# Kernel optimization log

Hardware: AMD Instinct MI355X
Metric: run time of the kernel (lower is better)

The kernel has to match this reference:

```python
import jax, jax.numpy as jnp
import numpy as np
import math

N = 50000
E = 800000
C_IN = 32
C_H = 256
C_OUT = 3
DEPTH = 3
RATIO = 0.5


def setup_inputs() -> dict:
    key = jax.random.key(0)
    ks = jax.random.split(key, 16)
    s = 0.05  # keep tanh/relu in a healthy range
    f32 = jnp.float32
    return {
        "x": jax.random.normal(ks[0], (N, C_IN), f32),
        "edge_index": jax.random.randint(ks[1], (2, E), 0, N, jnp.int32).astype(jnp.int64),
        "w0_l": jax.random.normal(ks[2], (C_IN, C_H), f32) * s,
        "w0_r": jax.random.normal(ks[3], (C_IN, C_H), f32) * s,
        "b0": jax.random.normal(ks[4], (C_H,), f32) * s,
        "dwl": jax.random.normal(ks[5], (DEPTH, C_H, C_H), f32) * s,
        "dwr": jax.random.normal(ks[6], (DEPTH, C_H, C_H), f32) * s,
        "db": jax.random.normal(ks[7], (DEPTH, C_H), f32) * s,
        "pool_w": jax.random.normal(ks[8], (DEPTH, C_H), f32),
        "uwl": jax.random.normal(ks[9], (DEPTH - 1, C_H, C_H), f32) * s,
        "uwr": jax.random.normal(ks[10], (DEPTH - 1, C_H, C_H), f32) * s,
        "ub": jax.random.normal(ks[11], (DEPTH - 1, C_H), f32) * s,
        "uwl_last": jax.random.normal(ks[12], (C_H, C_OUT), f32) * s,
        "uwr_last": jax.random.normal(ks[13], (C_H, C_OUT), f32) * s,
        "ub_last": jax.random.normal(ks[14], (C_OUT,), f32) * s,
    }


def _sage_max(x, src, dst, n, wl, wr, b):
    # SAGEConv(aggr='max'): out = lin_l(max_j x_j) + lin_r(x_i)
    # dst may contain dummy index n (masked edges); slice it off.
    msg = x[src]                                            # [E, C]
    agg = jax.ops.segment_max(msg, dst, num_segments=n + 1)[:n]
    agg = jnp.where(jnp.isfinite(agg), agg, 0.0)            # empty segments -> 0 (PyG)
    return agg @ wl + b + x @ wr


def _topk_pool(x, src, dst, w, ratio):
    # PyG TopKPooling with min_score=None: score=tanh((x.w)/||w||), keep top-k, rescale.
    n = x.shape[0]
    k = math.ceil(ratio * n)
    score = jnp.tanh((x @ w) / jnp.linalg.norm(w))          # [n]
    vals, perm = jax.lax.top_k(score, k)
    x2 = x[perm] * vals[:, None]
    # relabel edges; dropped edges -> dummy node k (fixed shape, equivalent for max-agg)
    mapping = jnp.full((n + 1,), -1, jnp.int32).at[perm].set(jnp.arange(k, dtype=jnp.int32))
    nsrc, ndst = mapping[src], mapping[dst]
    valid = (nsrc >= 0) & (ndst >= 0)
    src2 = jnp.where(valid, nsrc, 0)
    dst2 = jnp.where(valid, ndst, k)
    return x2, src2, dst2, perm, k


def reference(x, edge_index, w0_l, w0_r, b0, dwl, dwr, db, pool_w,
              uwl, uwr, ub, uwl_last, uwr_last, ub_last):
    n = x.shape[0]
    src = edge_index[0].astype(jnp.int32)
    dst = edge_index[1].astype(jnp.int32)

    x = jax.nn.relu(_sage_max(x, src, dst, n, w0_l, w0_r, b0))
    xs, srcs, dsts, ns, perms = [x], [src], [dst], [n], []

    for i in range(DEPTH):
        x, src, dst, perm, n = _topk_pool(x, src, dst, pool_w[i], RATIO)
        x = jax.nn.relu(_sage_max(x, src, dst, n, dwl[i], dwr[i], db[i]))
        if i < DEPTH - 1:
            xs.append(x); srcs.append(src); dsts.append(dst); ns.append(n)
        perms.append(perm)

    for i in range(DEPTH):
        j = DEPTH - 1 - i
        res, src, dst, n, perm = xs[j], srcs[j], dsts[j], ns[j], perms[j]
        up = jnp.zeros_like(res).at[perm].set(x)
        x = res + up                                         # sum_res=True
        if i < DEPTH - 1:
            x = jax.nn.relu(_sage_max(x, src, dst, n, uwl[i], uwr[i], ub[i]))
        else:
            x = _sage_max(x, src, dst, n, uwl_last, uwr_last, ub_last)

    return jnp.tanh(x) * 0.5
```

## Files before the change

### kernel.cpp

```cpp
#include <hip/hip_runtime.h>
#include <math.h>

#define E_NUM 800000
#define CH 256

typedef __attribute__((ext_vector_type(8))) short short8;
typedef __attribute__((ext_vector_type(4))) float float4v;

__device__ __forceinline__ unsigned f2key(float s) {
  unsigned b = __float_as_uint(s);
  return (b & 0x80000000u) ? ~b : (b | 0x80000000u);
}


__global__ __launch_bounds__(256) void k_deg(const int* __restrict__ dst, int n,
                                             int* __restrict__ deg) {
  int e = blockIdx.x * 256 + threadIdx.x;
  if (e < E_NUM) { int d = dst[e]; if (d < n) atomicAdd(&deg[d], 1); }
}

__global__ __launch_bounds__(256) void k_scan_block(const int* __restrict__ deg, int n,
                                                    int* __restrict__ incl,
                                                    int* __restrict__ bsum) {
  __shared__ int s[256];
  int i = blockIdx.x * 256 + threadIdx.x;
  int v = (i < n) ? deg[i] : 0;
  s[threadIdx.x] = v;
  __syncthreads();
  for (int o = 1; o < 256; o <<= 1) {
    int t = (threadIdx.x >= o) ? s[threadIdx.x - o] : 0;
    __syncthreads();
    s[threadIdx.x] += t;
    __syncthreads();
  }
  if (i < n) incl[i] = s[threadIdx.x];
  if (threadIdx.x == 255) bsum[blockIdx.x] = s[255];
}

__global__ void k_scan_bsum(int* bsum, int nb, int* total_out) {
  if (threadIdx.x == 0 && blockIdx.x == 0) {
    int acc = 0;
    for (int b = 0; b < nb; b++) { int v = bsum[b]; bsum[b] = acc; acc += v; }
    total_out[0] = acc;
  }
}

__global__ __launch_bounds__(256) void k_scan_final(const int* __restrict__ deg,
                                                    const int* __restrict__ incl,
                                                    const int* __restrict__ bsum, int n,
                                                    int* __restrict__ row,
                                                    int* __restrict__ cursor) {
  int i = blockIdx.x * 256 + threadIdx.x;
  if (i < n) {
    int r = incl[i] - deg[i] + bsum[blockIdx.x];
    row[i] = r;
    cursor[i] = r;
  }
}

__global__ __launch_bounds__(256) void k_fill(const int* __restrict__ src,
                                              const int* __restrict__ dst, int n,
                                              int* __restrict__ cursor,
                                              int* __restrict__ col) {
  int e = blockIdx.x * 256 + threadIdx.x;
  if (e < E_NUM) {
    int d = dst[e];
    if (d < n) { int p = atomicAdd(&cursor[d], 1); col[p] = src[e]; }
  }
}

__global__ __launch_bounds__(256) void k_relabel_deg(const int* __restrict__ srcIn,
                                                     const int* __restrict__ dstIn,
                                                     const int* __restrict__ mapping,
                                                     int kNew, int* __restrict__ srcOut,
                                                     int* __restrict__ dstOut,
                                                     int* __restrict__ deg) {
  int e = blockIdx.x * 256 + threadIdx.x;
  if (e >= E_NUM) return;
  int ns = mapping[srcIn[e]];
  int nd = mapping[dstIn[e]];
  if (ns >= 0 && nd >= 0) {
    srcOut[e] = ns;
    dstOut[e] = nd;
    atomicAdd(&deg[nd], 1);
  } else {
    srcOut[e] = 0;
    dstOut[e] = kNew;
  }
}


__device__ __forceinline__ float4 fmax4(float4 a, float4 b) {
  return make_float4(fmaxf(a.x, b.x), fmaxf(a.y, b.y), fmaxf(a.z, b.z), fmaxf(a.w, b.w));
}

__global__ __launch_bounds__(256) void k_aggmax32(const float* __restrict__ x,
                                                  const int* __restrict__ row,
                                                  const int* __restrict__ col,
                                                  float* __restrict__ out, int n) {
  int node = blockIdx.x * 8 + threadIdx.x / 32;
  int c = threadIdx.x % 32;
  if (node >= n) return;
  int e0 = row[node], e1 = row[node + 1];
  float m0 = -INFINITY, m1 = -INFINITY, m2 = -INFINITY, m3 = -INFINITY;
  int e = e0;
  for (; e + 4 <= e1; e += 4) {
    int s0 = col[e], s1 = col[e + 1], s2 = col[e + 2], s3 = col[e + 3];
    float v0 = x[(size_t)s0 * 32 + c];
    float v1 = x[(size_t)s1 * 32 + c];
    float v2 = x[(size_t)s2 * 32 + c];
    float v3 = x[(size_t)s3 * 32 + c];
    m0 = fmaxf(m0, v0); m1 = fmaxf(m1, v1); m2 = fmaxf(m2, v2); m3 = fmaxf(m3, v3);
  }
  for (; e < e1; e++) m0 = fmaxf(m0, x[(size_t)col[e] * 32 + c]);
  float m = fmaxf(fmaxf(m0, m1), fmaxf(m2, m3));
  out[(size_t)node * 32 + c] = (e1 > e0) ? m : 0.0f;
}

__global__ __launch_bounds__(256) void k_aggmax4(const float* __restrict__ x,
                                                 const int* __restrict__ row,
                                                 const int* __restrict__ col,
                                                 float* __restrict__ out, int n) {
  int lane = threadIdx.x & 63;
  int node = blockIdx.x * 4 + (threadIdx.x >> 6);
  if (node >= n) return;
  int e0 = row[node], e1 = row[node + 1];
  float4 m0 = make_float4(-INFINITY, -INFINITY, -INFINITY, -INFINITY);
  float4 m1 = m0, m2 = m0, m3 = m0;
  int e = e0;
  for (; e + 4 <= e1; e += 4) {
    int s0 = col[e], s1 = col[e + 1], s2 = col[e + 2], s3 = col[e + 3];
    float4 v0 = *(const float4*)&x[(size_t)s0 * CH + lane * 4];
    float4 v1 = *(const float4*)&x[(size_t)s1 * CH + lane * 4];
    float4 v2 = *(const float4*)&x[(size_t)s2 * CH + lane * 4];
    float4 v3 = *(const float4*)&x[(size_t)s3 * CH + lane * 4];
    m0 = fmax4(m0, v0); m1 = fmax4(m1, v1); m2 = fmax4(m2, v2); m3 = fmax4(m3, v3);
  }
  for (; e < e1; e++)
    m0 = fmax4(m0, *(const float4*)&x[(size_t)col[e] * CH + lane * 4]);
  float4 m = fmax4(fmax4(m0, m1), fmax4(m2, m3));
  if (e1 <= e0) m = make_float4(0.f, 0.f, 0.f, 0.f);
  *(float4*)&out[(size_t)node * CH + lane * 4] = m;
}

__device__ __forceinline__ float b2f(unsigned short s) {
  return __uint_as_float(((unsigned)s) << 16);
}
__device__ __forceinline__ float4 bmax4(float4 m, ushort4 v) {
  m.x = fmaxf(m.x, b2f(v.x));
  m.y = fmaxf(m.y, b2f(v.y));
  m.z = fmaxf(m.z, b2f(v.z));
  m.w = fmaxf(m.w, b2f(v.w));
  return m;
}

__global__ __launch_bounds__(256) void k_aggmax4_b16(const unsigned short* __restrict__ xb,
                                                     const int* __restrict__ row,
                                                     const int* __restrict__ col,
                                                     float* __restrict__ out, int n) {
  int lane = threadIdx.x & 63;
  int node = blockIdx.x * 4 + (threadIdx.x >> 6);
  if (node >= n) return;
  int e0 = row[node], e1 = row[node + 1];
  float4 m0 = make_float4(-INFINITY, -INFINITY, -INFINITY, -INFINITY);
  float4 m1 = m0, m2 = m0, m3 = m0;
  int e = e0;
  for (; e + 4 <= e1; e += 4) {
    int s0 = col[e], s1 = col[e + 1], s2 = col[e + 2], s3 = col[e + 3];
    ushort4 v0 = *(const ushort4*)&xb[(size_t)s0 * CH + lane * 4];
    ushort4 v1 = *(const ushort4*)&xb[(size_t)s1 * CH + lane * 4];
    ushort4 v2 = *(const ushort4*)&xb[(size_t)s2 * CH + lane * 4];
    ushort4 v3 = *(const ushort4*)&xb[(size_t)s3 * CH + lane * 4];
    m0 = bmax4(m0, v0); m1 = bmax4(m1, v1); m2 = bmax4(m2, v2); m3 = bmax4(m3, v3);
  }
  for (; e < e1; e++)
    m0 = bmax4(m0, *(const ushort4*)&xb[(size_t)col[e] * CH + lane * 4]);
  float4 m = fmax4(fmax4(m0, m1), fmax4(m2, m3));
  if (e1 <= e0) m = make_float4(0.f, 0.f, 0.f, 0.f);
  *(float4*)&out[(size_t)node * CH + lane * 4] = m;
}


__global__ __launch_bounds__(256) void k_wprep(const float* __restrict__ src,
                                               unsigned short* __restrict__ dst, int K,
                                               int nmat) {
  int idx = blockIdx.x * 256 + threadIdx.x;
  int total = nmat * K * 256;
  if (idx >= total) return;
  int n = idx % 256;
  int k = (idx / 256) % K;
  int m = idx / (256 * K);
  float v = src[idx];
  unsigned u = __float_as_uint(v);
  unsigned h = u & 0xFFFF0000u;
  float r = v - __uint_as_float(h);
  unsigned short hs = (unsigned short)(h >> 16);
  unsigned short ls = (unsigned short)(__float_as_uint(r) >> 16);
  int ib = k >> 5, kk = k & 31;
  size_t base = (size_t)m * 2 * K * 256;
  size_t o = ((size_t)ib * 256 + n) * 32 + kk;
  dst[base + o] = hs;
  dst[base + (size_t)K * 256 + o] = ls;
}


#define KSTR 40

__global__ __launch_bounds__(256) void k_gemm_mfma(
    const float* __restrict__ A1, const float* __restrict__ A2,
    const unsigned short* __restrict__ W1t, const unsigned short* __restrict__ W2t,
    const float* __restrict__ bias, float* __restrict__ out, int M, int K, int scatter,
    const int* __restrict__ perm, const float* __restrict__ scw,
    float* __restrict__ score, unsigned* __restrict__ hist1) {
  __shared__ unsigned short As_h[64 * KSTR], As_l[64 * KSTR];
  __shared__ unsigned short Bs_h[256 * KSTR], Bs_l[256 * KSTR];
  __shared__ float sred[4][64];
  const int t = threadIdx.x;
  const int wave = t >> 6, lane = t & 63;
  const int l15 = lane & 15, qd = lane >> 4;
  const int bm0 = blockIdx.x * 64;
  float4v acc[4][4];
#pragma unroll
  for (int a = 0; a < 4; a++)
#pragma unroll
    for (int b = 0; b < 4; b++) acc[a][b] = (float4v)0.f;
  const int sa_m = t >> 2;
  const int sa_kc = (t & 3) * 8;
  const int rok = (bm0 + sa_m) < M;
  const int nIb = K >> 5;
  for (int ib = 0; ib < 2 * nIb; ib++) {
    const float* A = (ib < nIb) ? A1 : A2;
    const unsigned short* Wt = (ib < nIb) ? W1t : W2t;
    int ib0 = (ib < nIb) ? ib : ib - nIb;
    float va[8];
    {
      const float* ap = &A[(size_t)(bm0 + sa_m) * K + (ib0 << 5) + sa_kc];
      float4 v0 = rok ? *(const float4*)ap : make_float4(0, 0, 0, 0);
      float4 v1 = rok ? *(const float4*)(ap + 4) : make_float4(0, 0, 0, 0);
      va[0] = v0.x; va[1] = v0.y; va[2] = v0.z; va[3] = v0.w;
      va[4] = v1.x; va[5] = v1.y; va[6] = v1.z; va[7] = v1.w;
    }
    unsigned hp[4], lp[4];
#pragma unroll
    for (int e = 0; e < 4; e++) {
      unsigned u0 = __float_as_uint(va[2 * e]);
      unsigned u1 = __float_as_uint(va[2 * e + 1]);
      unsigned h0 = u0 & 0xFFFF0000u, h1 = u1 & 0xFFFF0000u;
      float r0 = va[2 * e] - __uint_as_float(h0);
      float r1 = va[2 * e + 1] - __uint_as_float(h1);
      hp[e] = (h0 >> 16) | h1;
      lp[e] = (__float_as_uint(r0) >> 16) | (__float_as_uint(r1) & 0xFFFF0000u);
    }
    size_t ro = ((size_t)ib0 * 256 + t) * 32;
    uint4 bh0 = *(const uint4*)&Wt[ro];
    uint4 bh1 = *(const uint4*)&Wt[ro + 8];
    uint4 bh2 = *(const uint4*)&Wt[ro + 16];
    uint4 bh3 = *(const uint4*)&Wt[ro + 24];
    size_t rl = (size_t)K * 256 + ro;
    uint4 bl0 = *(const uint4*)&Wt[rl];
    uint4 bl1 = *(const uint4*)&Wt[rl + 8];
    uint4 bl2 = *(const uint4*)&Wt[rl + 16];
    uint4 bl3 = *(const uint4*)&Wt[rl + 24];
    __syncthreads();
    *(uint4*)&As_h[sa_m * KSTR + sa_kc] = make_uint4(hp[0], hp[1], hp[2], hp[3]);
    *(uint4*)&As_l[sa_m * KSTR + sa_kc] = make_uint4(lp[0], lp[1], lp[2], lp[3]);
    *(uint4*)&Bs_h[t * KSTR + 0] = bh0;
    *(uint4*)&Bs_h[t * KSTR + 8] = bh1;
    *(uint4*)&Bs_h[t * KSTR + 16] = bh2;
    *(uint4*)&Bs_h[t * KSTR + 24] = bh3;
    *(uint4*)&Bs_l[t * KSTR + 0] = bl0;
    *(uint4*)&Bs_l[t * KSTR + 8] = bl1;
    *(uint4*)&Bs_l[t * KSTR + 16] = bl2;
    *(uint4*)&Bs_l[t * KSTR + 24] = bl3;
    __syncthreads();
    short8 ah[4], al[4], bh[4], bl[4];
#pragma unroll
    for (int mt = 0; mt < 4; mt++) {
      int r = (mt * 16 + l15) * KSTR + qd * 8;
      ah[mt] = *(const short8*)&As_h[r];
      al[mt] = *(const short8*)&As_l[r];
    }
#pragma unroll
    for (int nt = 0; nt < 4; nt++) {
      int r = (wave * 64 + nt * 16 + l15) * KSTR + qd * 8;
      bh[nt] = *(const short8*)&Bs_h[r];
      bl[nt] = *(const short8*)&Bs_l[r];
    }
#pragma unroll
    for (int mt = 0; mt < 4; mt++)
#pragma unroll
      for (int nt = 0; nt < 4; nt++) {
        acc[mt][nt] =
            __builtin_amdgcn_mfma_f32_16x16x32_bf16(ah[mt], bh[nt], acc[mt][nt], 0, 0, 0);
        acc[mt][nt] =
            __builtin_amdgcn_mfma_f32_16x16x32_bf16(ah[mt], bl[nt], acc[mt][nt], 0, 0, 0);
        acc[mt][nt] =
            __builtin_amdgcn_mfma_f32_16x16x32_bf16(al[mt], bh[nt], acc[mt][nt], 0, 0, 0);
      }
  }
  const int col0 = wave * 64;
  if (scw) {
    if (t < 64) { sred[0][t] = 0.f; sred[1][t] = 0.f; sred[2][t] = 0.f; sred[3][t] = 0.f; }
    __syncthreads();
  }
#pragma unroll
  for (int mt = 0; mt < 4; mt++) {
    int rbase = mt * 16 + qd * 4;
    float sp[4] = {0.f, 0.f, 0.f, 0.f};
#pragma unroll
    for (int nt = 0; nt < 4; nt++) {
      int col = col0 + nt * 16 + l15;
      float bb = bias[col];
      float wc = scw ? scw[col] : 0.f;
#pragma unroll
      for (int r = 0; r < 4; r++) {
        int p = bm0 + rbase + r;
        if (p < M) {
          float v = fmaxf(acc[mt][nt][r] + bb, 0.f);
          if (scatter) {
            float* dp = &out[(size_t)perm[p] * CH + col];
            *dp += v;
          } else {
            out[(size_t)p * CH + col] = v;
            sp[r] += v * wc;
          }
        }
      }
    }
    if (scw) {
#pragma unroll
      for (int r = 0; r < 4; r++) {
        float s = sp[r];
#pragma unroll
        for (int o = 1; o < 16; o <<= 1) s += __shfl_xor(s, o);
        if (l15 == 0) sred[wave][rbase + r] = s;
      }
    }
  }
  if (scw) {
    __syncthreads();
    if (t < 64 && bm0 + t < M) {
      float s = sred[0][t] + sred[1][t] + sred[2][t] + sred[3][t];
      score[bm0 + t] = s;
      atomicAdd(&hist1[f2key(s) >> 16], 1u);
    }
  }
}


__global__ __launch_bounds__(1024) void k_resolve(const unsigned* __restrict__ hist,
                                                  unsigned* __restrict__ state, int pass,
                                                  int k0) {
  __shared__ unsigned csum[1024];
  int t = threadIdx.x;
  int base = 65535 - 64 * t;
  unsigned s = 0;
  for (int j = 0; j < 64; j++) s += hist[base - j];
  csum[t] = s;
  __syncthreads();
  for (int o = 1; o < 1024; o <<= 1) {
    unsigned v = (t >= o) ? csum[t - o] : 0u;
    __syncthreads();
    csum[t] += v;
    __syncthreads();
  }
  unsigned cumBefore = csum[t] - s;
  unsigned kneed = (pass == 0) ? (unsigned)k0 : state[5];
  if (cumBefore < kneed && kneed <= cumBefore + s) {
    unsigned cum = cumBefore;
    for (int j = 0; j < 64; j++) {
      unsigned c = hist[base - j];
      if (cum + c >= kneed) {
        unsigned bucket = (unsigned)(base - j);
        if (pass == 0) {
          state[4] = bucket;
          state[5] = kneed - cum;
        } else {
          state[0] = (state[4] << 16) | bucket;
          state[1] = kneed - cum;
          state[2] = 0u;
          state[3] = 0u;
        }
        break;
      }
      cum += c;
    }
  }
}

__global__ __launch_bounds__(256) void k_hist2(const float* __restrict__ score, int n,
                                               const unsigned* __restrict__ state,
                                               unsigned* __restrict__ hist2) {
  int i = blockIdx.x * 256 + threadIdx.x;
  if (i >= n) return;
  unsigned u = f2key(score[i]);
  if ((u >> 16) == state[4]) atomicAdd(&hist2[u & 0xFFFFu], 1u);
}

__global__ __launch_bounds__(256) void k_compact(const float* __restrict__ score, int n,
                                                 unsigned* __restrict__ state,
                                                 int* __restrict__ perm,
                                                 int* __restrict__ mapping) {
  int i = blockIdx.x * 256 + threadIdx.x;
  if (i > n) return;
  if (i == n) { mapping[n] = -1; return; }
  unsigned Kth = state[0];
  unsigned kneed = state[1];
  unsigned u = f2key(score[i]);
  int m = -1;
  if (u > Kth) {
    unsigned p = atomicAdd(&state[2], 1u);
    perm[p] = i;
    m = (int)p;
  } else if (u == Kth) {
    unsigned tt = atomicAdd(&state[3], 1u);
    if (tt < kneed) {
      unsigned p = atomicAdd(&state[2], 1u);
      perm[p] = i;
      m = (int)p;
    }
  }
  mapping[i] = m;
}

__global__ __launch_bounds__(256) void k_gather(const float* __restrict__ x,
                                                const int* __restrict__ perm,
                                                const float* __restrict__ score,
                                                const float* __restrict__ pw,
                                                float* __restrict__ out, int k) {
  int lane = threadIdx.x & 63;
  int node = blockIdx.x * 4 + (threadIdx.x >> 6);
  float4 w4 = *(const float4*)&pw[lane * 4];
  float nn = w4.x * w4.x + w4.y * w4.y + w4.z * w4.z + w4.w * w4.w;
#pragma unroll
  for (int o = 32; o > 0; o >>= 1) nn += __shfl_down(nn, o);
  nn = __shfl(nn, 0);
  if (node >= k) return;
  int i = perm[node];
  float tv = tanhf(score[i] / sqrtf(nn));
  float4 v = *(const float4*)&x[(size_t)i * CH + lane * 4];
  v.x *= tv; v.y *= tv; v.z *= tv; v.w *= tv;
  *(float4*)&out[(size_t)node * CH + lane * 4] = v;
}


__device__ __forceinline__ unsigned short f2b_rn(float f) {
  unsigned u = __float_as_uint(f);
  u += 0x7FFFu + ((u >> 16) & 1u);
  return (unsigned short)(u >> 16);
}

__global__ __launch_bounds__(256) void k_cvtb16(const float* __restrict__ x,
                                                unsigned short* __restrict__ xb, int n) {
  int lane = threadIdx.x & 63;
  int node = blockIdx.x * 4 + (threadIdx.x >> 6);
  if (node >= n) return;
  float4 a = *(const float4*)&x[(size_t)node * CH + lane * 4];
  ushort4 o;
  o.x = f2b_rn(a.x); o.y = f2b_rn(a.y); o.z = f2b_rn(a.z); o.w = f2b_rn(a.w);
  *(ushort4*)&xb[(size_t)node * CH + lane * 4] = o;
}

__global__ __launch_bounds__(256) void k_final(const unsigned short* __restrict__ XB,
                                               const int* __restrict__ row,
                                               const int* __restrict__ col,
                                               const float* __restrict__ wl,
                                               const float* __restrict__ wr,
                                               const float* __restrict__ b,
                                               float* __restrict__ out, int n) {
  int lane = threadIdx.x & 63;
  int node = blockIdx.x * 4 + (threadIdx.x >> 6);
  if (node >= n) return;
  int e0 = row[node], e1 = row[node + 1];
  float4 m0 = make_float4(-INFINITY, -INFINITY, -INFINITY, -INFINITY);
  float4 m1 = m0, m2 = m0, m3 = m0;
  int e = e0;
  for (; e + 4 <= e1; e += 4) {
    int s0 = col[e], s1 = col[e + 1], s2 = col[e + 2], s3 = col[e + 3];
    ushort4 v0 = *(const ushort4*)&XB[(size_t)s0 * CH + lane * 4];
    ushort4 v1 = *(const ushort4*)&XB[(size_t)s1 * CH + lane * 4];
    ushort4 v2 = *(const ushort4*)&XB[(size_t)s2 * CH + lane * 4];
    ushort4 v3 = *(const ushort4*)&XB[(size_t)s3 * CH + lane * 4];
    m0 = bmax4(m0, v0); m1 = bmax4(m1, v1); m2 = bmax4(m2, v2); m3 = bmax4(m3, v3);
  }
  for (; e < e1; e++)
    m0 = bmax4(m0, *(const ushort4*)&XB[(size_t)col[e] * CH + lane * 4]);
  float4 m = fmax4(fmax4(m0, m1), fmax4(m2, m3));
  if (e1 <= e0) m = make_float4(0.f, 0.f, 0.f, 0.f);
  ushort4 sv4 = *(const ushort4*)&XB[(size_t)node * CH + lane * 4];
  float wlv[12], wrv[12];
  *(float4*)&wlv[0] = ((const float4*)(wl + 12 * lane))[0];
  *(float4*)&wlv[4] = ((const float4*)(wl + 12 * lane))[1];
  *(float4*)&wlv[8] = ((const float4*)(wl + 12 * lane))[2];
  *(float4*)&wrv[0] = ((const float4*)(wr + 12 * lane))[0];
  *(float4*)&wrv[4] = ((const float4*)(wr + 12 * lane))[1];
  *(float4*)&wrv[8] = ((const float4*)(wr + 12 * lane))[2];
  float av[4] = {m.x, m.y, m.z, m.w};
  float sv[4] = {b2f(sv4.x), b2f(sv4.y), b2f(sv4.z), b2f(sv4.w)};
  float p[3] = {0.f, 0.f, 0.f};
#pragma unroll
  for (int q = 0; q < 4; q++)
#pragma unroll
    for (int jj = 0; jj < 3; jj++)
      p[jj] += av[q] * wlv[q * 3 + jj] + sv[q] * wrv[q * 3 + jj];
#pragma unroll
  for (int jj = 0; jj < 3; jj++) {
#pragma unroll
    for (int o = 32; o > 0; o >>= 1) p[jj] += __shfl_down(p[jj], o);
  }
  if (lane == 0) {
#pragma unroll
    for (int jj = 0; jj < 3; jj++)
      out[(size_t)node * 3 + jj] = tanhf(p[jj] + b[jj]) * 0.5f;
  }
}


extern "C" void kernel_launch(void* const* d_in, const int* in_sizes, int n_in,
                              void* d_out, int out_size, void* d_ws, size_t ws_size,
                              hipStream_t stream) {
  (void)in_sizes; (void)n_in; (void)out_size; (void)ws_size;
  const float* xin = (const float*)d_in[0];
  const int* ei = (const int*)d_in[1];
  const int* src0 = ei;
  const int* dst0 = ei + E_NUM;
  const float* w0l = (const float*)d_in[2];
  const float* w0r = (const float*)d_in[3];
  const float* b0 = (const float*)d_in[4];
  const float* dwl = (const float*)d_in[5];
  const float* dwr = (const float*)d_in[6];
  const float* db = (const float*)d_in[7];
  const float* poolw = (const float*)d_in[8];
  const float* uwl = (const float*)d_in[9];
  const float* uwr = (const float*)d_in[10];
  const float* ub = (const float*)d_in[11];
  const float* uwlL = (const float*)d_in[12];
  const float* uwrL = (const float*)d_in[13];
  const float* ubL = (const float*)d_in[14];
  float* out = (float*)d_out;

  char* base = (char*)d_ws;
  size_t off = 0;
  auto alloc = [&](size_t bytes) -> void* {
    void* p = base + off;
    off = (off + bytes + 255) & ~(size_t)255;
    return p;
  };

  const int n0 = 50000, n1 = 25000, n2 = 12500, n3 = 6250;
  float* X0 = (float*)alloc((size_t)n0 * CH * 4);
  float* X1 = (float*)alloc((size_t)n1 * CH * 4);
  float* X2 = (float*)alloc((size_t)n2 * CH * 4);
  float* AGG = (float*)alloc((size_t)n1 * CH * 4);
  float* PD = (float*)alloc((size_t)n1 * CH * 4);
  unsigned short* XB = (unsigned short*)alloc((size_t)n0 * CH * 2);
  unsigned short* X1B = (unsigned short*)alloc((size_t)n1 * CH * 2);
  unsigned short* X2B = (unsigned short*)alloc((size_t)n2 * CH * 2);
  int* eA = (int*)alloc((size_t)2 * E_NUM * 4);
  int* eB = (int*)alloc((size_t)2 * E_NUM * 4);
  int* col0 = (int*)alloc((size_t)E_NUM * 4);
  int* col1 = (int*)alloc((size_t)E_NUM * 4);
  int* col2 = (int*)alloc((size_t)E_NUM * 4);
  int* col3 = (int*)alloc((size_t)E_NUM * 4);
  int* row0 = (int*)alloc((size_t)(n0 + 1) * 4);
  int* row1 = (int*)alloc((size_t)(n1 + 1) * 4);
  int* row2 = (int*)alloc((size_t)(n2 + 1) * 4);
  int* row3 = (int*)alloc((size_t)(n3 + 1) * 4);
  int* map1 = (int*)alloc((size_t)(n0 + 1) * 4);
  int* map2 = (int*)alloc((size_t)(n1 + 1) * 4);
  int* map3 = (int*)alloc((size_t)(n2 + 1) * 4);
  int* perm1 = (int*)alloc((size_t)n1 * 4);
  int* perm2 = (int*)alloc((size_t)n2 * 4);
  int* perm3 = (int*)alloc((size_t)n3 * 4);
  float* score = (float*)alloc((size_t)n0 * 4);
  int* deg = (int*)alloc((size_t)n0 * 4);
  int* incl = (int*)alloc((size_t)n0 * 4);
  int* cursor = (int*)alloc((size_t)n0 * 4);
  int* bsum = (int*)alloc((size_t)256 * 4);
  unsigned* state = (unsigned*)alloc(1024);
  unsigned* hist = (unsigned*)alloc((size_t)2 * 65536 * 4);
  const size_t WSZ = (size_t)2 * 256 * 256;
  unsigned short* Wt0l = (unsigned short*)alloc((size_t)2 * 32 * 256 * 2);
  unsigned short* Wt0r = (unsigned short*)alloc((size_t)2 * 32 * 256 * 2);
  unsigned short* Wtdl = (unsigned short*)alloc(3 * WSZ * 2);
  unsigned short* Wtdr = (unsigned short*)alloc(3 * WSZ * 2);
  unsigned short* Wtul = (unsigned short*)alloc(2 * WSZ * 2);
  unsigned short* Wtur = (unsigned short*)alloc(2 * WSZ * 2);

  const int EG = (E_NUM + 255) / 256;

  k_wprep<<<(32 * 256 + 255) / 256, 256, 0, stream>>>(w0l, Wt0l, 32, 1);
  k_wprep<<<(32 * 256 + 255) / 256, 256, 0, stream>>>(w0r, Wt0r, 32, 1);
  k_wprep<<<(3 * 256 * 256 + 255) / 256, 256, 0, stream>>>(dwl, Wtdl, 256, 3);
  k_wprep<<<(3 * 256 * 256 + 255) / 256, 256, 0, stream>>>(dwr, Wtdr, 256, 3);
  k_wprep<<<(2 * 256 * 256 + 255) / 256, 256, 0, stream>>>(uwl, Wtul, 256, 2);
  k_wprep<<<(2 * 256 * 256 + 255) / 256, 256, 0, stream>>>(uwr, Wtur, 256, 2);

  auto csrRest = [&](const int* esrc, const int* edst, int n, int* rowp, int* colp) {
    int nb = (n + 255) / 256;
    k_scan_block<<<nb, 256, 0, stream>>>(deg, n, incl, bsum);
    k_scan_bsum<<<1, 1, 0, stream>>>(bsum, nb, rowp + n);
    k_scan_final<<<nb, 256, 0, stream>>>(deg, incl, bsum, n, rowp, cursor);
    k_fill<<<EG, 256, 0, stream>>>(esrc, edst, n, cursor, colp);
  };

  auto poolLevel = [&](const float* X, const float* pw, int n, int k, int* mapping,
                       int* permL, const int* esrcIn, const int* edstIn, int* esrcOut,
                       int* edstOut, float* Pout) {
    k_resolve<<<1, 1024, 0, stream>>>(hist, state, 0, k);
    k_hist2<<<(n + 255) / 256, 256, 0, stream>>>(score, n, state, hist + 65536);
    k_resolve<<<1, 1024, 0, stream>>>(hist + 65536, state, 1, k);
    k_compact<<<(n + 1 + 255) / 256, 256, 0, stream>>>(score, n, state, permL, mapping);
    k_gather<<<(k + 3) / 4, 256, 0, stream>>>(X, permL, score, pw, Pout, k);
    hipMemsetAsync(deg, 0, (size_t)k * 4, stream);
    k_relabel_deg<<<EG, 256, 0, stream>>>(esrcIn, edstIn, mapping, k, esrcOut, edstOut,
                                          deg);
  };

  auto gemm = [&](const float* A1, const float* A2, const unsigned short* W1t,
                  const unsigned short* W2t, const float* bias, float* o, int M, int K,
                  int scatter, const int* prm, const float* scw, float* sc) {
    if (scw) hipMemsetAsync(hist, 0, (size_t)2 * 65536 * 4, stream);
    k_gemm_mfma<<<(M + 63) / 64, 256, 0, stream>>>(A1, A2, W1t, W2t, bias, o, M, K,
                                                   scatter, prm, scw, sc, hist);
  };

  hipMemsetAsync(deg, 0, (size_t)n0 * 4, stream);
  k_deg<<<EG, 256, 0, stream>>>(dst0, n0, deg);
  csrRest(src0, dst0, n0, row0, col0);
  k_aggmax32<<<(n0 + 7) / 8, 256, 0, stream>>>(xin, row0, col0, AGG, n0);
  gemm(AGG, xin, Wt0l, Wt0r, b0, X0, n0, 32, 0, nullptr, poolw + 0 * CH, score);

  poolLevel(X0, poolw + 0 * CH, n0, n1, map1, perm1, src0, dst0, eA, eA + E_NUM, PD);
  csrRest(eA, eA + E_NUM, n1, row1, col1);
  k_aggmax4<<<(n1 + 3) / 4, 256, 0, stream>>>(PD, row1, col1, AGG, n1);
  gemm(AGG, PD, Wtdl + 0 * WSZ, Wtdr + 0 * WSZ, db + 0 * CH, X1, n1, 256, 0, nullptr,
       poolw + 1 * CH, score);

  poolLevel(X1, poolw + 1 * CH, n1, n2, map2, perm2, eA, eA + E_NUM, eB, eB + E_NUM, PD);
  csrRest(eB, eB + E_NUM, n2, row2, col2);
  k_aggmax4<<<(n2 + 3) / 4, 256, 0, stream>>>(PD, row2, col2, AGG, n2);
  gemm(AGG, PD, Wtdl + 1 * WSZ, Wtdr + 1 * WSZ, db + 1 * CH, X2, n2, 256, 0, nullptr,
       poolw + 2 * CH, score);

  poolLevel(X2, poolw + 2 * CH, n2, n3, map3, perm3, eB, eB + E_NUM, eA, eA + E_NUM, PD);
  csrRest(eA, eA + E_NUM, n3, row3, col3);
  k_aggmax4<<<(n3 + 3) / 4, 256, 0, stream>>>(PD, row3, col3, AGG, n3);
  gemm(AGG, PD, Wtdl + 2 * WSZ, Wtdr + 2 * WSZ, db + 2 * CH, X2, n3, 256, 1, perm3,
       nullptr, nullptr);

  k_cvtb16<<<(n2 + 3) / 4, 256, 0, stream>>>(X2, X2B, n2);
  k_aggmax4_b16<<<(n2 + 3) / 4, 256, 0, stream>>>(X2B, row2, col2, AGG, n2);
  gemm(AGG, X2, Wtul + 0 * WSZ, Wtur + 0 * WSZ, ub + 0 * CH, X1, n2, 256, 1, perm2,
       nullptr, nullptr);

  k_cvtb16<<<(n1 + 3) / 4, 256, 0, stream>>>(X1, X1B, n1);
  k_aggmax4_b16<<<(n1 + 3) / 4, 256, 0, stream>>>(X1B, row1, col1, AGG, n1);
  gemm(AGG, X1, Wtul + 1 * WSZ, Wtur + 1 * WSZ, ub + 1 * CH, X0, n1, 256, 1, perm1,
       nullptr, nullptr);

  k_cvtb16<<<(n0 + 3) / 4, 256, 0, stream>>>(X0, XB, n0);
  k_final<<<(n0 + 3) / 4, 256, 0, stream>>>(XB, row0, col0, uwlL, uwrL, ubL, out, n0);
}
```

Before: 973.1 us.

## Compact surviving edges after pooling and vectorize GEMM epilogue stores

Edge relabeling now appends only surviving edges to the output arrays, using a global atomic counter. Later CSR fill and relabel kernels read that device-side count and exit early for edges beyond it, so dropped edges are no longer processed at deeper levels. Separately, the MFMA operands are swapped so each lane holds four consecutive output columns. This lets the GEMM epilogue load bias and score weights as float4, use float4 stores and read-modify-writes, and shrink the score reduction to two shuffles. The trade-off is a contended single-address atomic for edge compaction and grids still sized for the full edge count.

```diff
diff --git a/kernel.cpp b/kernel.cpp
--- a/kernel.cpp
+++ b/kernel.cpp
@@ -59,33 +59,36 @@
 }
 
 __global__ __launch_bounds__(256) void k_fill(const int* __restrict__ src,
-                                              const int* __restrict__ dst, int n,
+                                              const int* __restrict__ dst,
+                                              const int* __restrict__ ecnt,
                                               int* __restrict__ cursor,
                                               int* __restrict__ col) {
   int e = blockIdx.x * 256 + threadIdx.x;
-  if (e < E_NUM) {
-    int d = dst[e];
-    if (d < n) { int p = atomicAdd(&cursor[d], 1); col[p] = src[e]; }
-  }
+  int ne = ecnt ? *ecnt : E_NUM;
+  if (e >= ne) return;
+  int d = dst[e];
+  int p = atomicAdd(&cursor[d], 1);
+  col[p] = src[e];
 }
 
 __global__ __launch_bounds__(256) void k_relabel_deg(const int* __restrict__ srcIn,
                                                      const int* __restrict__ dstIn,
+                                                     const int* __restrict__ ecntIn,
                                                      const int* __restrict__ mapping,
-                                                     int kNew, int* __restrict__ srcOut,
+                                                     int* __restrict__ srcOut,
                                                      int* __restrict__ dstOut,
-                                                     int* __restrict__ deg) {
+                                                     int* __restrict__ deg,
+                                                     int* __restrict__ ecntOut) {
   int e = blockIdx.x * 256 + threadIdx.x;
-  if (e >= E_NUM) return;
+  int ne = ecntIn ? *ecntIn : E_NUM;
+  if (e >= ne) return;
   int ns = mapping[srcIn[e]];
   int nd = mapping[dstIn[e]];
   if (ns >= 0 && nd >= 0) {
-    srcOut[e] = ns;
-    dstOut[e] = nd;
+    int p = atomicAdd(ecntOut, 1);
+    srcOut[p] = ns;
+    dstOut[p] = nd;
     atomicAdd(&deg[nd], 1);
-  } else {
-    srcOut[e] = 0;
-    dstOut[e] = kNew;
   }
 }
 
@@ -291,11 +294,11 @@
 #pragma unroll
       for (int nt = 0; nt < 4; nt++) {
         acc[mt][nt] =
-            __builtin_amdgcn_mfma_f32_16x16x32_bf16(ah[mt], bh[nt], acc[mt][nt], 0, 0, 0);
+            __builtin_amdgcn_mfma_f32_16x16x32_bf16(bh[nt], ah[mt], acc[mt][nt], 0, 0, 0);
         acc[mt][nt] =
-            __builtin_amdgcn_mfma_f32_16x16x32_bf16(ah[mt], bl[nt], acc[mt][nt], 0, 0, 0);
+            __builtin_amdgcn_mfma_f32_16x16x32_bf16(bl[nt], ah[mt], acc[mt][nt], 0, 0, 0);
         acc[mt][nt] =
-            __builtin_amdgcn_mfma_f32_16x16x32_bf16(al[mt], bh[nt], acc[mt][nt], 0, 0, 0);
+            __builtin_amdgcn_mfma_f32_16x16x32_bf16(bh[nt], al[mt], acc[mt][nt], 0, 0, 0);
       }
   }
   const int col0 = wave * 64;
@@ -303,38 +306,51 @@
     if (t < 64) { sred[0][t] = 0.f; sred[1][t] = 0.f; sred[2][t] = 0.f; sred[3][t] = 0.f; }
     __syncthreads();
   }
+  float bias4[4][4], scw4[4][4];
+#pragma unroll
+  for (int nt = 0; nt < 4; nt++) {
+    int cb = col0 + nt * 16 + qd * 4;
+    *(float4*)bias4[nt] = *(const float4*)&bias[cb];
+    if (scw) *(float4*)scw4[nt] = *(const float4*)&scw[cb];
+  }
 #pragma unroll
   for (int mt = 0; mt < 4; mt++) {
-    int rbase = mt * 16 + qd * 4;
-    float sp[4] = {0.f, 0.f, 0.f, 0.f};
-#pragma unroll
-    for (int nt = 0; nt < 4; nt++) {
-      int col = col0 + nt * 16 + l15;
-      float bb = bias[col];
-      float wc = scw ? scw[col] : 0.f;
-#pragma unroll
-      for (int r = 0; r < 4; r++) {
-        int p = bm0 + rbase + r;
-        if (p < M) {
-          float v = fmaxf(acc[mt][nt][r] + bb, 0.f);
-          if (scatter) {
-            float* dp = &out[(size_t)perm[p] * CH + col];
-            *dp += v;
-          } else {
-            out[(size_t)p * CH + col] = v;
-            sp[r] += v * wc;
-          }
+    int p = bm0 + mt * 16 + l15;
+    float sp = 0.f;
+    if (p < M) {
+      if (scatter) {
+        size_t rb = (size_t)perm[p] * CH + col0 + qd * 4;
+#pragma unroll
+        for (int nt = 0; nt < 4; nt++) {
+          float* dp = &out[rb + nt * 16];
+          float4 old = *(const float4*)dp;
+          float4 v;
+          v.x = old.x + fmaxf(acc[mt][nt][0] + bias4[nt][0], 0.f);
+          v.y = old.y + fmaxf(acc[mt][nt][1] + bias4[nt][1], 0.f);
+          v.z = old.z + fmaxf(acc[mt][nt][2] + bias4[nt][2], 0.f);
+          v.w = old.w + fmaxf(acc[mt][nt][3] + bias4[nt][3], 0.f);
+          *(float4*)dp = v;
+        }
+      } else {
+        size_t rb = (size_t)p * CH + col0 + qd * 4;
+#pragma unroll
+        for (int nt = 0; nt < 4; nt++) {
+          float4 v;
+          v.x = fmaxf(acc[mt][nt][0] + bias4[nt][0], 0.f);
+          v.y = fmaxf(acc[mt][nt][1] + bias4[nt][1], 0.f);
+          v.z = fmaxf(acc[mt][nt][2] + bias4[nt][2], 0.f);
+          v.w = fmaxf(acc[mt][nt][3] + bias4[nt][3], 0.f);
+          *(float4*)&out[rb + nt * 16] = v;
+          if (scw)
+            sp += v.x * scw4[nt][0] + v.y * scw4[nt][1] + v.z * scw4[nt][2] +
+                  v.w * scw4[nt][3];
         }
       }
     }
     if (scw) {
-#pragma unroll
-      for (int r = 0; r < 4; r++) {
-        float s = sp[r];
-#pragma unroll
-        for (int o = 1; o < 16; o <<= 1) s += __shfl_xor(s, o);
-        if (l15 == 0) sred[wave][rbase + r] = s;
-      }
+      sp += __shfl_xor(sp, 16);
+      sp += __shfl_xor(sp, 32);
+      if (qd == 0) sred[wave][mt * 16 + l15] = sp;
     }
   }
   if (scw) {
@@ -577,6 +593,7 @@
   int* incl = (int*)alloc((size_t)n0 * 4);
   int* cursor = (int*)alloc((size_t)n0 * 4);
   int* bsum = (int*)alloc((size_t)256 * 4);
+  int* ecnt = (int*)alloc((size_t)4 * 4);
   unsigned* state = (unsigned*)alloc(1024);
   unsigned* hist = (unsigned*)alloc((size_t)2 * 65536 * 4);
   const size_t WSZ = (size_t)2 * 256 * 256;
@@ -596,25 +613,28 @@
   k_wprep<<<(2 * 256 * 256 + 255) / 256, 256, 0, stream>>>(uwl, Wtul, 256, 2);
   k_wprep<<<(2 * 256 * 256 + 255) / 256, 256, 0, stream>>>(uwr, Wtur, 256, 2);
 
-  auto csrRest = [&](const int* esrc, const int* edst, int n, int* rowp, int* colp) {
+  auto csrRest = [&](const int* esrc, const int* edst, const int* ec, int n, int* rowp,
+                     int* colp) {
     int nb = (n + 255) / 256;
     k_scan_block<<<nb, 256, 0, stream>>>(deg, n, incl, bsum);
     k_scan_bsum<<<1, 1, 0, stream>>>(bsum, nb, rowp + n);
     k_scan_final<<<nb, 256, 0, stream>>>(deg, incl, bsum, n, rowp, cursor);
-    k_fill<<<EG, 256, 0, stream>>>(esrc, edst, n, cursor, colp);
+    k_fill<<<EG, 256, 0, stream>>>(esrc, edst, ec, cursor, colp);
   };
 
   auto poolLevel = [&](const float* X, const float* pw, int n, int k, int* mapping,
-                       int* permL, const int* esrcIn, const int* edstIn, int* esrcOut,
-                       int* edstOut, float* Pout) {
+                       int* permL, const int* esrcIn, const int* edstIn,
+                       const int* ecntIn, int* esrcOut, int* edstOut, int* ecntOut,
+                       float* Pout) {
     k_resolve<<<1, 1024, 0, stream>>>(hist, state, 0, k);
     k_hist2<<<(n + 255) / 256, 256, 0, stream>>>(score, n, state, hist + 65536);
     k_resolve<<<1, 1024, 0, stream>>>(hist + 65536, state, 1, k);
     k_compact<<<(n + 1 + 255) / 256, 256, 0, stream>>>(score, n, state, permL, mapping);
     k_gather<<<(k + 3) / 4, 256, 0, stream>>>(X, permL, score, pw, Pout, k);
     hipMemsetAsync(deg, 0, (size_t)k * 4, stream);
-    k_relabel_deg<<<EG, 256, 0, stream>>>(esrcIn, edstIn, mapping, k, esrcOut, edstOut,
-                                          deg);
+    hipMemsetAsync(ecntOut, 0, 4, stream);
+    k_relabel_deg<<<EG, 256, 0, stream>>>(esrcIn, edstIn, ecntIn, mapping, esrcOut,
+                                          edstOut, deg, ecntOut);
   };
 
   auto gemm = [&](const float* A1, const float* A2, const unsigned short* W1t,
@@ -627,24 +647,27 @@
 
   hipMemsetAsync(deg, 0, (size_t)n0 * 4, stream);
   k_deg<<<EG, 256, 0, stream>>>(dst0, n0, deg);
-  csrRest(src0, dst0, n0, row0, col0);
+  csrRest(src0, dst0, nullptr, n0, row0, col0);
   k_aggmax32<<<(n0 + 7) / 8, 256, 0, stream>>>(xin, row0, col0, AGG, n0);
   gemm(AGG, xin, Wt0l, Wt0r, b0, X0, n0, 32, 0, nullptr, poolw + 0 * CH, score);
 
-  poolLevel(X0, poolw + 0 * CH, n0, n1, map1, perm1, src0, dst0, eA, eA + E_NUM, PD);
-  csrRest(eA, eA + E_NUM, n1, row1, col1);
+  poolLevel(X0, poolw + 0 * CH, n0, n1, map1, perm1, src0, dst0, nullptr, eA, eA + E_NUM,
+            ecnt + 0, PD);
+  csrRest(eA, eA + E_NUM, ecnt + 0, n1, row1, col1);
   k_aggmax4<<<(n1 + 3) / 4, 256, 0, stream>>>(PD, row1, col1, AGG, n1);
   gemm(AGG, PD, Wtdl + 0 * WSZ, Wtdr + 0 * WSZ, db + 0 * CH, X1, n1, 256, 0, nullptr,
        poolw + 1 * CH, score);
 
-  poolLevel(X1, poolw + 1 * CH, n1, n2, map2, perm2, eA, eA + E_NUM, eB, eB + E_NUM, PD);
-  csrRest(eB, eB + E_NUM, n2, row2, col2);
+  poolLevel(X1, poolw + 1 * CH, n1, n2, map2, perm2, eA, eA + E_NUM, ecnt + 0, eB,
+            eB + E_NUM, ecnt + 1, PD);
+  csrRest(eB, eB + E_NUM, ecnt + 1, n2, row2, col2);
   k_aggmax4<<<(n2 + 3) / 4, 256, 0, stream>>>(PD, row2, col2, AGG, n2);
   gemm(AGG, PD, Wtdl + 1 * WSZ, Wtdr + 1 * WSZ, db + 1 * CH, X2, n2, 256, 0, nullptr,
        poolw + 2 * CH, score);
 
-  poolLevel(X2, poolw + 2 * CH, n2, n3, map3, perm3, eB, eB + E_NUM, eA, eA + E_NUM, PD);
-  csrRest(eA, eA + E_NUM, n3, row3, col3);
+  poolLevel(X2, poolw + 2 * CH, n2, n3, map3, perm3, eB, eB + E_NUM, ecnt + 1, eA,
+            eA + E_NUM, ecnt + 2, PD);
+  csrRest(eA, eA + E_NUM, ecnt + 2, n3, row3, col3);
   k_aggmax4<<<(n3 + 3) / 4, 256, 0, stream>>>(PD, row3, col3, AGG, n3);
   gemm(AGG, PD, Wtdl + 2 * WSZ, Wtdr + 2 * WSZ, db + 2 * CH, X2, n3, 256, 1, perm3,
        nullptr, nullptr);
```

After: 1.048 ms. 7.7% more time.
